# Kernel tuning notes

Measured on AMD Instinct MI355X. Metric: run time of the kernel, lower is better.

## Reference

```python
import jax, jax.numpy as jnp
import numpy as np

B, S, IN, H = 256, 512, 512, 512

def setup_inputs() -> dict:
    key = jax.random.key(0)
    ks = jax.random.split(key, 8)
    s = 1.0 / np.sqrt(H)
    si = 1.0 / np.sqrt(IN)
    return {
        "inputs": jax.random.normal(ks[0], (B, S, IN), dtype=jnp.float32),
        "timestamps": jax.random.uniform(ks[1], (B, S), dtype=jnp.float32),
        "W_all_w": jax.random.uniform(ks[2], (4 * H, H), dtype=jnp.float32, minval=-s, maxval=s),
        "W_all_b": jax.random.uniform(ks[3], (4 * H,), dtype=jnp.float32, minval=-s, maxval=s),
        "U_all_w": jax.random.uniform(ks[4], (4 * H, IN), dtype=jnp.float32, minval=-si, maxval=si),
        "U_all_b": jax.random.uniform(ks[5], (4 * H,), dtype=jnp.float32, minval=-si, maxval=si),
        "W_d_w": jax.random.uniform(ks[6], (H, H), dtype=jnp.float32, minval=-s, maxval=s),
        "W_d_b": jax.random.uniform(ks[7], (H,), dtype=jnp.float32, minval=-s, maxval=s),
    }

def reference(inputs, timestamps, W_all_w, W_all_b, U_all_w, U_all_b, W_d_w, W_d_b):
    b, seq, _ = inputs.shape
    hsz = W_d_w.shape[0]
    # Precompute input projections for all steps at once: [B,S,4H]
    u_proj = jnp.einsum('bsi,gi->bsg', inputs, U_all_w) + U_all_b

    def step(carry, xs):
        h, c = carry
        u_t, t_t = xs  # u_t: [B,4H], t_t: [B]
        c_s1 = jnp.tanh(c @ W_d_w.T + W_d_b)
        c_adj = c - c_s1 + c_s1 * t_t[:, None]
        outs = h @ W_all_w.T + W_all_b + u_t
        f, i, o, c_tmp = jnp.split(outs, 4, axis=1)
        f = jax.nn.sigmoid(f)
        i = jax.nn.sigmoid(i)
        o = jax.nn.sigmoid(o)
        c_tmp = jnp.tanh(c_tmp)
        c = f * c_adj + i * c_tmp
        h = o * jnp.tanh(c)
        return (h, c), (o, h, c)

    h0 = jnp.zeros((b, hsz), dtype=inputs.dtype)
    c0 = jnp.zeros((b, hsz), dtype=inputs.dtype)
    (h, c), (o_seq, h_seq, c_seq) = jax.lax.scan(
        step, (h0, c0),
        (jnp.swapaxes(u_proj, 0, 1), jnp.swapaxes(timestamps, 0, 1)))
    outputs = jnp.swapaxes(o_seq, 0, 1)  # [B,S,H]
    return outputs, h, c
```

## Files before the change

### kernel.cpp

```cpp
#include <hip/hip_runtime.h>
#include <hip/hip_bf16.h>
#include <math.h>

#define BATCH 256
#define SEQ   512
#define IN_D  512
#define HID   512
#define FOURH 2048
#define BS_ROWS (BATCH * SEQ)

typedef __bf16 bf16x8 __attribute__((ext_vector_type(8)));
typedef float  f32x4  __attribute__((ext_vector_type(4)));
typedef unsigned long long ull;

__device__ __forceinline__ float sigf(float x)  { return 1.0f / (1.0f + __expf(-x)); }
__device__ __forceinline__ float tanhf_(float x){ return 1.0f - 2.0f / (__expf(2.0f * x) + 1.0f); }

__global__ __launch_bounds__(256) void init_kernel(
    const float* __restrict__ W_all_w, const float* __restrict__ W_all_b,
    const float* __restrict__ U_all_w, const float* __restrict__ U_all_b,
    const float* __restrict__ W_d_w,
    __bf16* __restrict__ Wb, __bf16* __restrict__ Ub, __bf16* __restrict__ Db,
    float* __restrict__ bias_all,
    unsigned* __restrict__ hc,
    unsigned* __restrict__ bar)
{
    const int stride = gridDim.x * blockDim.x;
    const int tid0 = blockIdx.x * blockDim.x + threadIdx.x;

    const int nW = FOURH * HID;
    for (int i = tid0; i < nW; i += stride) {
        Wb[i] = (__bf16)W_all_w[i];
        Ub[i] = (__bf16)U_all_w[i];
    }
    const int nD = HID * HID;
    for (int i = tid0; i < nD; i += stride) Db[i] = (__bf16)W_d_w[i];
    for (int i = tid0; i < FOURH; i += stride) bias_all[i] = W_all_b[i] + U_all_b[i];
    for (int i = tid0; i < 2 * BATCH * HID; i += stride) hc[i] = 0u;
    for (int i = tid0; i < 256 * 32; i += stride) bar[i] = 0u;
}

__global__ __launch_bounds__(256) void uproj_gemm(
    const float* __restrict__ x, const __bf16* __restrict__ Ub,
    __bf16* __restrict__ up)
{
    const unsigned bid = blockIdx.x;
    const unsigned lg = (bid & 7) * 2048u + (bid >> 3);
    const int cb = lg & 15;
    const int rb = lg >> 4;

    __shared__ __bf16 As[128][64];
    __shared__ __bf16 Bs[128][64];

    const int tid = threadIdx.x;
    const int wave = tid >> 6, lane = tid & 63;
    const int wm = wave >> 1, wn = wave & 1;
    const int lrow = lane & 15, kq = lane >> 4;
    const int sw = (lrow & 7) << 3;

    f32x4 acc[4][4];
    #pragma unroll
    for (int m = 0; m < 4; ++m)
        #pragma unroll
        for (int n = 0; n < 4; ++n) acc[m][n] = (f32x4){0.f, 0.f, 0.f, 0.f};

    const int srow = tid >> 1;
    const int skc  = (tid & 1) * 32;
    const int dsw  = (srow & 7) << 3;

    for (int kk = 0; kk < 512; kk += 64) {
        {
            const float* xs = x + (size_t)(rb * 128 + srow) * 512 + kk + skc;
            #pragma unroll
            for (int j = 0; j < 4; ++j) {
                float4 va = ((const float4*)xs)[2 * j];
                float4 vb = ((const float4*)xs)[2 * j + 1];
                bf16x8 pk;
                pk[0] = (__bf16)va.x; pk[1] = (__bf16)va.y;
                pk[2] = (__bf16)va.z; pk[3] = (__bf16)va.w;
                pk[4] = (__bf16)vb.x; pk[5] = (__bf16)vb.y;
                pk[6] = (__bf16)vb.z; pk[7] = (__bf16)vb.w;
                *(bf16x8*)&As[srow][(skc + j * 8) ^ dsw] = pk;
            }
            const __bf16* bsrc = Ub + (size_t)(cb * 128 + srow) * 512 + kk + skc;
            #pragma unroll
            for (int j = 0; j < 4; ++j)
                *(uint4*)&Bs[srow][(skc + j * 8) ^ dsw] = *(const uint4*)(bsrc + j * 8);
        }
        __syncthreads();

        #pragma unroll
        for (int k2 = 0; k2 < 2; ++k2) {
            const int ke = k2 * 32 + kq * 8;
            bf16x8 af[4], bfr[4];
            #pragma unroll
            for (int m = 0; m < 4; ++m)
                af[m] = *(const bf16x8*)&As[wm * 64 + m * 16 + lrow][ke ^ sw];
            #pragma unroll
            for (int n = 0; n < 4; ++n)
                bfr[n] = *(const bf16x8*)&Bs[wn * 64 + n * 16 + lrow][ke ^ sw];
            #pragma unroll
            for (int m = 0; m < 4; ++m)
                #pragma unroll
                for (int n = 0; n < 4; ++n)
                    acc[m][n] = __builtin_amdgcn_mfma_f32_16x16x32_bf16(af[m], bfr[n], acc[m][n], 0, 0, 0);
        }
        __syncthreads();
    }

    const int colL = lane & 15, r0 = (lane >> 4) * 4;
    const size_t orow0 = (size_t)rb * 128 + wm * 64;
    const int ocol0 = cb * 128 + wn * 64;
    #pragma unroll
    for (int m = 0; m < 4; ++m)
        #pragma unroll
        for (int n = 0; n < 4; ++n)
            #pragma unroll
            for (int i = 0; i < 4; ++i)
                up[(orow0 + m * 16 + r0 + i) * 2048 + ocol0 + n * 16 + colL] = (__bf16)acc[m][n][i];
}

__global__ __launch_bounds__(512) void scan_kernel(
    const __bf16* __restrict__ up,
    const float* __restrict__ timestamps,
    const __bf16* __restrict__ Wb,
    const __bf16* __restrict__ Db,
    const float* __restrict__ bias_all,
    const float* __restrict__ Wd_b,
    unsigned* __restrict__ hc,
    unsigned* __restrict__ bar,
    float* __restrict__ out)
{
    const int tid = threadIdx.x;
    const int bid = blockIdx.x;
    const int bg = bid & 7, hcid = bid >> 3;
    const int b0 = bg * 32;
    const int k0 = hcid * 16;
    const int wave = tid >> 6, lane = tid & 63;
    const int lrow = lane & 15, kq = lane >> 4;
    const int sw = (lrow & 7) << 3;

    __shared__ __bf16 Ah[32][512];
    __shared__ __bf16 Ac[32][512];
    __shared__ float  exg[4 * 2 * 32 * 16];
    __shared__ float  exd[4 * 32 * 16];
    __shared__ __bf16 Us[2][32][64];
    __shared__ float  Ts[2][32];
    __shared__ float  Cm[512];
    __shared__ float  BiasW[64];
    __shared__ float  BiasD[16];

    bf16x8 Bg[2][8];
    bf16x8 Bd[4];
    if (wave < 4) {
        const int kh = wave & 1, pb = wave >> 1;
        #pragma unroll
        for (int uu = 0; uu < 2; ++uu) {
            const int u = pb * 2 + uu;
            #pragma unroll
            for (int ks = 0; ks < 8; ++ks) {
                const int kk = kh * 256 + ks * 32 + kq * 8;
                Bg[uu][ks] = *(const bf16x8*)(Wb + (size_t)(u * 512 + k0 + lrow) * 512 + kk);
            }
        }
    } else {
        const int kq4 = wave - 4;
        #pragma unroll
        for (int ks = 0; ks < 4; ++ks) {
            const int kk = kq4 * 128 + ks * 32 + kq * 8;
            Bd[ks] = *(const bf16x8*)(Db + (size_t)(k0 + lrow) * 512 + kk);
        }
    }

    if (tid < 64) BiasW[tid] = bias_all[(tid >> 4) * 512 + k0 + (tid & 15)];
    else if (tid < 80) BiasD[tid - 64] = Wd_b[k0 + (tid - 64)];
    Cm[tid] = 0.f;
    if (tid < 256) {
        const int row = tid >> 3, j = tid & 7;
        const __bf16* src = up + ((size_t)(b0 + row) * 512 + 0) * 2048
                               + (j >> 1) * 512 + k0 + (j & 1) * 8;
        *(uint4*)&Us[0][row][(j >> 1) * 16 + (j & 1) * 8] = *(const uint4*)src;
    }
    if (tid < 32) Ts[0][tid] = timestamps[(size_t)(b0 + tid) * 512 + 0];
    __syncthreads();

    #pragma unroll 1
    for (int t = 0; t < SEQ; ++t) {
        const int par = t & 1;

        if (t > 0) {
            if (tid < 32) {
                unsigned* fl = &bar[(bg * 32 + tid) * 32];
                while (__hip_atomic_load(fl, __ATOMIC_RELAXED,
                                         __HIP_MEMORY_SCOPE_AGENT) < (unsigned)t)
                    __builtin_amdgcn_s_sleep(2);
            }
            __syncthreads();
        }

        {
            const ull* src = (const ull*)(hc + (size_t)par * BATCH * HID + b0 * 512);
            ull v[16];
            #pragma unroll
            for (int i = 0; i < 16; ++i)
                v[i] = __hip_atomic_load(src + i * 512 + tid, __ATOMIC_RELAXED,
                                         __HIP_MEMORY_SCOPE_AGENT);
            #pragma unroll
            for (int i = 0; i < 16; ++i) {
                const int g = i * 512 + tid;
                const int row = g >> 8;
                const int cp = (g & 255) * 2;
                const unsigned lo = (unsigned)v[i];
                const unsigned hi = (unsigned)(v[i] >> 32);
                const unsigned hp = (lo & 0xFFFFu) | (hi << 16);
                const unsigned cpk = (lo >> 16) | (hi & 0xFFFF0000u);
                const int d = cp ^ ((row & 7) << 3);
                *(unsigned*)&Ah[row][d] = hp;
                *(unsigned*)&Ac[row][d] = cpk;
            }
        }
        __syncthreads();

        uint4 upf;
        float tpf = 0.f;
        const bool do_pf = (t + 1 < SEQ);
        if (do_pf && tid >= 256) {
            const int row = (tid - 256) >> 3, j = (tid - 256) & 7;
            upf = *(const uint4*)(up + ((size_t)(b0 + row) * 512 + (t + 1)) * 2048
                                  + (j >> 1) * 512 + k0 + (j & 1) * 8);
            if (tid < 288) tpf = timestamps[(size_t)(b0 + (tid - 256)) * 512 + (t + 1)];
        }

        if (wave < 4) {
            const int kh = wave & 1, pb = wave >> 1;
            f32x4 acc[2][2];
            #pragma unroll
            for (int uu = 0; uu < 2; ++uu)
                #pragma unroll
                for (int rh = 0; rh < 2; ++rh) acc[uu][rh] = (f32x4){0.f, 0.f, 0.f, 0.f};
            #pragma unroll
            for (int ks = 0; ks < 8; ++ks) {
                const int koff = (kh * 256 + ks * 32 + kq * 8) ^ sw;
                bf16x8 a0 = *(const bf16x8*)&Ah[lrow][koff];
                bf16x8 a1 = *(const bf16x8*)&Ah[16 + lrow][koff];
                #pragma unroll
                for (int uu = 0; uu < 2; ++uu) {
                    acc[uu][0] = __builtin_amdgcn_mfma_f32_16x16x32_bf16(a0, Bg[uu][ks], acc[uu][0], 0, 0, 0);
                    acc[uu][1] = __builtin_amdgcn_mfma_f32_16x16x32_bf16(a1, Bg[uu][ks], acc[uu][1], 0, 0, 0);
                }
            }
            const int colL = lane & 15, r0 = (lane >> 4) * 4;
            #pragma unroll
            for (int uu = 0; uu < 2; ++uu)
                #pragma unroll
                for (int rh = 0; rh < 2; ++rh)
                    #pragma unroll
                    for (int i = 0; i < 4; ++i)
                        exg[(((pb * 2 + uu) * 2 + kh) * 32 + rh * 16 + r0 + i) * 16 + colL] = acc[uu][rh][i];
        } else {
            const int kq4 = wave - 4;
            f32x4 acc0 = {0.f, 0.f, 0.f, 0.f}, acc1 = {0.f, 0.f, 0.f, 0.f};
            #pragma unroll
            for (int ks = 0; ks < 4; ++ks) {
                const int koff = (kq4 * 128 + ks * 32 + kq * 8) ^ sw;
                bf16x8 a0 = *(const bf16x8*)&Ac[lrow][koff];
                bf16x8 a1 = *(const bf16x8*)&Ac[16 + lrow][koff];
                acc0 = __builtin_amdgcn_mfma_f32_16x16x32_bf16(a0, Bd[ks], acc0, 0, 0, 0);
                acc1 = __builtin_amdgcn_mfma_f32_16x16x32_bf16(a1, Bd[ks], acc1, 0, 0, 0);
            }
            const int colL = lane & 15, r0 = (lane >> 4) * 4;
            #pragma unroll
            for (int i = 0; i < 4; ++i) {
                exd[(kq4 * 32 + r0 + i) * 16 + colL]      = acc0[i];
                exd[(kq4 * 32 + 16 + r0 + i) * 16 + colL] = acc1[i];
            }
        }

        if (do_pf && tid >= 256) {
            const int row = (tid - 256) >> 3, j = (tid - 256) & 7;
            *(uint4*)&Us[par ^ 1][row][(j >> 1) * 16 + (j & 1) * 8] = upf;
            if (tid < 288) Ts[par ^ 1][tid - 256] = tpf;
        }
        __syncthreads();

        float o_def = 0.f;
        {
            const int r = tid >> 4, k = tid & 15;
            float g4[4];
            #pragma unroll
            for (int g = 0; g < 4; ++g)
                g4[g] = exg[((g * 2 + 0) * 32 + r) * 16 + k]
                      + exg[((g * 2 + 1) * 32 + r) * 16 + k]
                      + (float)Us[par][r][g * 16 + k] + BiasW[g * 16 + k];
            float dd = BiasD[k];
            #pragma unroll
            for (int q = 0; q < 4; ++q) dd += exd[(q * 32 + r) * 16 + k];

            const float c_old = Cm[tid];
            const float tt = Ts[par][r];
            const float c_s1  = tanhf_(dd);
            const float c_adj = c_old - c_s1 + c_s1 * tt;
            const float f  = sigf(g4[0]);
            const float ii = sigf(g4[1]);
            const float o  = sigf(g4[2]);
            const float c_tmp = tanhf_(g4[3]);
            const float c_new = f * c_adj + ii * c_tmp;
            const float h_new = o * tanhf_(c_new);
            Cm[tid] = c_new;

            if (t == SEQ - 1) {
                __builtin_nontemporal_store(o,
                    &out[((size_t)(b0 + r) * 512 + t) * 512 + k0 + k]);
                const size_t base = (size_t)BATCH * SEQ * HID;
                out[base + (size_t)(b0 + r) * 512 + k0 + k] = h_new;
                out[base + (size_t)BATCH * HID + (size_t)(b0 + r) * 512 + k0 + k] = c_new;
            } else {
                o_def = o;
                const unsigned short hb = __builtin_bit_cast(unsigned short, (__bf16)h_new);
                const unsigned short cb = __builtin_bit_cast(unsigned short, (__bf16)c_new);
                const unsigned pk = (unsigned)hb | ((unsigned)cb << 16);
                unsigned* dst = hc + (size_t)(par ^ 1) * BATCH * HID
                                   + (size_t)(b0 + r) * 512 + k0 + k;
                __hip_atomic_store(dst, pk, __ATOMIC_RELAXED, __HIP_MEMORY_SCOPE_AGENT);
            }
        }
        __syncthreads();

        if (t < SEQ - 1) {
            if (tid == 0)
                __hip_atomic_store(&bar[(bg * 32 + hcid) * 32], (unsigned)(t + 1),
                                   __ATOMIC_RELAXED, __HIP_MEMORY_SCOPE_AGENT);
            {
                const int r = tid >> 4, k = tid & 15;
                __builtin_nontemporal_store(o_def,
                    &out[((size_t)(b0 + r) * 512 + t) * 512 + k0 + k]);
            }
        }
    }
}

extern "C" void kernel_launch(void* const* d_in, const int* in_sizes, int n_in,
                              void* d_out, int out_size, void* d_ws, size_t ws_size,
                              hipStream_t stream) {
    const float* inputs     = (const float*)d_in[0];
    const float* timestamps = (const float*)d_in[1];
    const float* W_all_w    = (const float*)d_in[2];
    const float* W_all_b    = (const float*)d_in[3];
    const float* U_all_w    = (const float*)d_in[4];
    const float* U_all_b    = (const float*)d_in[5];
    const float* W_d_w      = (const float*)d_in[6];
    const float* W_d_b      = (const float*)d_in[7];
    float* out = (float*)d_out;

    char* ws = (char*)d_ws;
    size_t off = 0;
    auto alloc = [&](size_t bytes) -> void* {
        void* p = ws + off;
        off += (bytes + 255) & ~(size_t)255;
        return p;
    };
    __bf16* Wb       = (__bf16*)alloc((size_t)FOURH * HID * 2);
    __bf16* Ub       = (__bf16*)alloc((size_t)FOURH * HID * 2);
    __bf16* Db       = (__bf16*)alloc((size_t)HID * HID * 2);
    float*  bias_all = (float*) alloc((size_t)FOURH * 4);
    unsigned* hcbuf  = (unsigned*)alloc((size_t)2 * BATCH * HID * 4);
    unsigned* bar    = (unsigned*)alloc(256 * 32 * 4);
    __bf16* up       = (__bf16*)alloc((size_t)BS_ROWS * FOURH * 2);

    hipLaunchKernelGGL(init_kernel, dim3(1024), dim3(256), 0, stream,
                       W_all_w, W_all_b, U_all_w, U_all_b, W_d_w,
                       Wb, Ub, Db, bias_all, hcbuf, bar);

    hipLaunchKernelGGL(uproj_gemm, dim3(16384), dim3(256), 0, stream,
                       inputs, Ub, up);

    void* sargs[] = {
        (void*)&up, (void*)&timestamps, (void*)&Wb, (void*)&Db,
        (void*)&bias_all, (void*)&W_d_b,
        (void*)&hcbuf, (void*)&bar, (void*)&out
    };
    hipLaunchCooperativeKernel((const void*)scan_kernel, dim3(256), dim3(512),
                               sargs, 0, stream);
}
```

Measured before the change: 2.585 ms.

## Load recurrent h/c fragments directly from global into MFMA registers, skipping LDS staging

The scan kernel now stores h and c in separate bf16 buffers and has every wave load its MFMA A-fragments straight from global memory into registers. This removes the per-step LDS staging copy and the extra barrier that went with it. The work is also redistributed so all 8 waves handle both the gate GEMM and the decay GEMM, split over K quarters and row halves, and the exchange arrays are padded to stride 17 to avoid bank conflicts. The trade-offs are more global loads per step, more partial sums to reduce, and h/c stores paired through lane shuffles.

Result: slower. 3.784 ms (+46.4%).

```diff
diff --git a/kernel.cpp b/kernel.cpp
--- a/kernel.cpp
+++ b/kernel.cpp
@@ -11,10 +11,13 @@
 
 typedef __bf16 bf16x8 __attribute__((ext_vector_type(8)));
 typedef float  f32x4  __attribute__((ext_vector_type(4)));
+typedef unsigned uint32x4 __attribute__((ext_vector_type(4)));
 typedef unsigned long long ull;
 
 __device__ __forceinline__ float sigf(float x)  { return 1.0f / (1.0f + __expf(-x)); }
 __device__ __forceinline__ float tanhf_(float x){ return 1.0f - 2.0f / (__expf(2.0f * x) + 1.0f); }
+
+union frag_cvt { ull u[2]; bf16x8 v; };
 
 __global__ __launch_bounds__(256) void init_kernel(
     const float* __restrict__ W_all_w, const float* __restrict__ W_all_b,
@@ -22,7 +25,8 @@
     const float* __restrict__ W_d_w,
     __bf16* __restrict__ Wb, __bf16* __restrict__ Ub, __bf16* __restrict__ Db,
     float* __restrict__ bias_all,
-    unsigned* __restrict__ hc,
+    unsigned* __restrict__ hz,
+    unsigned* __restrict__ cz,
     unsigned* __restrict__ bar)
 {
     const int stride = gridDim.x * blockDim.x;
@@ -36,7 +40,8 @@
     const int nD = HID * HID;
     for (int i = tid0; i < nD; i += stride) Db[i] = (__bf16)W_d_w[i];
     for (int i = tid0; i < FOURH; i += stride) bias_all[i] = W_all_b[i] + U_all_b[i];
-    for (int i = tid0; i < 2 * BATCH * HID; i += stride) hc[i] = 0u;
+    const int nH = BATCH * HID;
+    for (int i = tid0; i < nH; i += stride) { hz[i] = 0u; cz[i] = 0u; }
     for (int i = tid0; i < 256 * 32; i += stride) bar[i] = 0u;
 }
 
@@ -127,7 +132,8 @@
     const __bf16* __restrict__ Db,
     const float* __restrict__ bias_all,
     const float* __restrict__ Wd_b,
-    unsigned* __restrict__ hc,
+    __bf16* __restrict__ hbuf,
+    __bf16* __restrict__ cbuf,
     unsigned* __restrict__ bar,
     float* __restrict__ out)
 {
@@ -138,39 +144,26 @@
     const int k0 = hcid * 16;
     const int wave = tid >> 6, lane = tid & 63;
     const int lrow = lane & 15, kq = lane >> 4;
-    const int sw = (lrow & 7) << 3;
-
-    __shared__ __bf16 Ah[32][512];
-    __shared__ __bf16 Ac[32][512];
-    __shared__ float  exg[4 * 2 * 32 * 16];
-    __shared__ float  exd[4 * 32 * 16];
+    const int rh = wave >> 2, kq4 = wave & 3;
+    const int kb = kq4 * 128 + kq * 8;
+
+    __shared__ float  exg[16 * 32 * 17];
+    __shared__ float  exd[4 * 32 * 17];
     __shared__ __bf16 Us[2][32][64];
     __shared__ float  Ts[2][32];
     __shared__ float  Cm[512];
     __shared__ float  BiasW[64];
     __shared__ float  BiasD[16];
 
-    bf16x8 Bg[2][8];
-    bf16x8 Bd[4];
-    if (wave < 4) {
-        const int kh = wave & 1, pb = wave >> 1;
-        #pragma unroll
-        for (int uu = 0; uu < 2; ++uu) {
-            const int u = pb * 2 + uu;
-            #pragma unroll
-            for (int ks = 0; ks < 8; ++ks) {
-                const int kk = kh * 256 + ks * 32 + kq * 8;
-                Bg[uu][ks] = *(const bf16x8*)(Wb + (size_t)(u * 512 + k0 + lrow) * 512 + kk);
-            }
-        }
-    } else {
-        const int kq4 = wave - 4;
-        #pragma unroll
-        for (int ks = 0; ks < 4; ++ks) {
-            const int kk = kq4 * 128 + ks * 32 + kq * 8;
-            Bd[ks] = *(const bf16x8*)(Db + (size_t)(k0 + lrow) * 512 + kk);
-        }
-    }
+    bf16x8 Bg[4][4], Bd4[4];
+    #pragma unroll
+    for (int u = 0; u < 4; ++u)
+        #pragma unroll
+        for (int ks = 0; ks < 4; ++ks)
+            Bg[u][ks] = *(const bf16x8*)(Wb + (size_t)(u * 512 + k0 + lrow) * 512 + kb + ks * 32);
+    #pragma unroll
+    for (int ks = 0; ks < 4; ++ks)
+        Bd4[ks] = *(const bf16x8*)(Db + (size_t)(k0 + lrow) * 512 + kb + ks * 32);
 
     if (tid < 64) BiasW[tid] = bias_all[(tid >> 4) * 512 + k0 + (tid & 15)];
     else if (tid < 80) BiasD[tid - 64] = Wd_b[k0 + (tid - 64)];
@@ -184,6 +177,8 @@
     if (tid < 32) Ts[0][tid] = timestamps[(size_t)(b0 + tid) * 512 + 0];
     __syncthreads();
 
+    const int arow = b0 + rh * 16 + lrow;
+
     #pragma unroll 1
     for (int t = 0; t < SEQ; ++t) {
         const int par = t & 1;
@@ -193,93 +188,67 @@
                 unsigned* fl = &bar[(bg * 32 + tid) * 32];
                 while (__hip_atomic_load(fl, __ATOMIC_RELAXED,
                                          __HIP_MEMORY_SCOPE_AGENT) < (unsigned)t)
-                    __builtin_amdgcn_s_sleep(2);
+                    __builtin_amdgcn_s_sleep(1);
             }
             __syncthreads();
         }
 
-        {
-            const ull* src = (const ull*)(hc + (size_t)par * BATCH * HID + b0 * 512);
-            ull v[16];
-            #pragma unroll
-            for (int i = 0; i < 16; ++i)
-                v[i] = __hip_atomic_load(src + i * 512 + tid, __ATOMIC_RELAXED,
-                                         __HIP_MEMORY_SCOPE_AGENT);
-            #pragma unroll
-            for (int i = 0; i < 16; ++i) {
-                const int g = i * 512 + tid;
-                const int row = g >> 8;
-                const int cp = (g & 255) * 2;
-                const unsigned lo = (unsigned)v[i];
-                const unsigned hi = (unsigned)(v[i] >> 32);
-                const unsigned hp = (lo & 0xFFFFu) | (hi << 16);
-                const unsigned cpk = (lo >> 16) | (hi & 0xFFFF0000u);
-                const int d = cp ^ ((row & 7) << 3);
-                *(unsigned*)&Ah[row][d] = hp;
-                *(unsigned*)&Ac[row][d] = cpk;
-            }
-        }
-        __syncthreads();
-
-        uint4 upf;
+        const __bf16* hs = hbuf + (size_t)par * BATCH * HID;
+        const __bf16* cs = cbuf + (size_t)par * BATCH * HID;
+        const size_t abase = (size_t)arow * 512 + kb;
+        ull ahv[4][2], acv[4][2];
+        #pragma unroll
+        for (int ks = 0; ks < 4; ++ks) {
+            const ull* ph = (const ull*)(hs + abase + ks * 32);
+            const ull* pc = (const ull*)(cs + abase + ks * 32);
+            ahv[ks][0] = __hip_atomic_load(ph,     __ATOMIC_RELAXED, __HIP_MEMORY_SCOPE_AGENT);
+            ahv[ks][1] = __hip_atomic_load(ph + 1, __ATOMIC_RELAXED, __HIP_MEMORY_SCOPE_AGENT);
+            acv[ks][0] = __hip_atomic_load(pc,     __ATOMIC_RELAXED, __HIP_MEMORY_SCOPE_AGENT);
+            acv[ks][1] = __hip_atomic_load(pc + 1, __ATOMIC_RELAXED, __HIP_MEMORY_SCOPE_AGENT);
+        }
+
+        uint32x4 upf;
         float tpf = 0.f;
         const bool do_pf = (t + 1 < SEQ);
-        if (do_pf && tid >= 256) {
-            const int row = (tid - 256) >> 3, j = (tid - 256) & 7;
-            upf = *(const uint4*)(up + ((size_t)(b0 + row) * 512 + (t + 1)) * 2048
-                                  + (j >> 1) * 512 + k0 + (j & 1) * 8);
-            if (tid < 288) tpf = timestamps[(size_t)(b0 + (tid - 256)) * 512 + (t + 1)];
-        }
-
-        if (wave < 4) {
-            const int kh = wave & 1, pb = wave >> 1;
-            f32x4 acc[2][2];
-            #pragma unroll
-            for (int uu = 0; uu < 2; ++uu)
+        if (do_pf && tid < 256) {
+            const int row = tid >> 3, j = tid & 7;
+            upf = __builtin_nontemporal_load(
+                (const uint32x4*)(up + ((size_t)(b0 + row) * 512 + (t + 1)) * 2048
+                                  + (j >> 1) * 512 + k0 + (j & 1) * 8));
+        }
+        if (do_pf && tid < 32) tpf = timestamps[(size_t)(b0 + tid) * 512 + (t + 1)];
+
+        f32x4 ag[4], ad;
+        #pragma unroll
+        for (int u = 0; u < 4; ++u) ag[u] = (f32x4){0.f, 0.f, 0.f, 0.f};
+        ad = (f32x4){0.f, 0.f, 0.f, 0.f};
+        #pragma unroll
+        for (int ks = 0; ks < 4; ++ks) {
+            frag_cvt fh; fh.u[0] = ahv[ks][0]; fh.u[1] = ahv[ks][1];
+            #pragma unroll
+            for (int u = 0; u < 4; ++u)
+                ag[u] = __builtin_amdgcn_mfma_f32_16x16x32_bf16(fh.v, Bg[u][ks], ag[u], 0, 0, 0);
+            frag_cvt fc; fc.u[0] = acv[ks][0]; fc.u[1] = acv[ks][1];
+            ad = __builtin_amdgcn_mfma_f32_16x16x32_bf16(fc.v, Bd4[ks], ad, 0, 0, 0);
+        }
+
+        if (do_pf && tid < 256) {
+            const int row = tid >> 3, j = tid & 7;
+            *(uint32x4*)&Us[par ^ 1][row][(j >> 1) * 16 + (j & 1) * 8] = upf;
+        }
+        if (do_pf && tid < 32) Ts[par ^ 1][tid] = tpf;
+
+        {
+            const int colL = lane & 15, r0 = (lane >> 4) * 4;
+            const int rbase = rh * 16 + r0;
+            #pragma unroll
+            for (int u = 0; u < 4; ++u)
                 #pragma unroll
-                for (int rh = 0; rh < 2; ++rh) acc[uu][rh] = (f32x4){0.f, 0.f, 0.f, 0.f};
-            #pragma unroll
-            for (int ks = 0; ks < 8; ++ks) {
-                const int koff = (kh * 256 + ks * 32 + kq * 8) ^ sw;
-                bf16x8 a0 = *(const bf16x8*)&Ah[lrow][koff];
-                bf16x8 a1 = *(const bf16x8*)&Ah[16 + lrow][koff];
-                #pragma unroll
-                for (int uu = 0; uu < 2; ++uu) {
-                    acc[uu][0] = __builtin_amdgcn_mfma_f32_16x16x32_bf16(a0, Bg[uu][ks], acc[uu][0], 0, 0, 0);
-                    acc[uu][1] = __builtin_amdgcn_mfma_f32_16x16x32_bf16(a1, Bg[uu][ks], acc[uu][1], 0, 0, 0);
-                }
-            }
-            const int colL = lane & 15, r0 = (lane >> 4) * 4;
-            #pragma unroll
-            for (int uu = 0; uu < 2; ++uu)
-                #pragma unroll
-                for (int rh = 0; rh < 2; ++rh)
-                    #pragma unroll
-                    for (int i = 0; i < 4; ++i)
-                        exg[(((pb * 2 + uu) * 2 + kh) * 32 + rh * 16 + r0 + i) * 16 + colL] = acc[uu][rh][i];
-        } else {
-            const int kq4 = wave - 4;
-            f32x4 acc0 = {0.f, 0.f, 0.f, 0.f}, acc1 = {0.f, 0.f, 0.f, 0.f};
-            #pragma unroll
-            for (int ks = 0; ks < 4; ++ks) {
-                const int koff = (kq4 * 128 + ks * 32 + kq * 8) ^ sw;
-                bf16x8 a0 = *(const bf16x8*)&Ac[lrow][koff];
-                bf16x8 a1 = *(const bf16x8*)&Ac[16 + lrow][koff];
-                acc0 = __builtin_amdgcn_mfma_f32_16x16x32_bf16(a0, Bd[ks], acc0, 0, 0, 0);
-                acc1 = __builtin_amdgcn_mfma_f32_16x16x32_bf16(a1, Bd[ks], acc1, 0, 0, 0);
-            }
-            const int colL = lane & 15, r0 = (lane >> 4) * 4;
-            #pragma unroll
-            for (int i = 0; i < 4; ++i) {
-                exd[(kq4 * 32 + r0 + i) * 16 + colL]      = acc0[i];
-                exd[(kq4 * 32 + 16 + r0 + i) * 16 + colL] = acc1[i];
-            }
-        }
-
-        if (do_pf && tid >= 256) {
-            const int row = (tid - 256) >> 3, j = (tid - 256) & 7;
-            *(uint4*)&Us[par ^ 1][row][(j >> 1) * 16 + (j & 1) * 8] = upf;
-            if (tid < 288) Ts[par ^ 1][tid - 256] = tpf;
+                for (int i = 0; i < 4; ++i)
+                    exg[((u * 4 + kq4) * 32 + rbase + i) * 17 + colL] = ag[u][i];
+            #pragma unroll
+            for (int i = 0; i < 4; ++i)
+                exd[(kq4 * 32 + rbase + i) * 17 + colL] = ad[i];
         }
         __syncthreads();
 
@@ -289,12 +258,14 @@
             float g4[4];
             #pragma unroll
             for (int g = 0; g < 4; ++g)
-                g4[g] = exg[((g * 2 + 0) * 32 + r) * 16 + k]
-                      + exg[((g * 2 + 1) * 32 + r) * 16 + k]
-                      + (float)Us[par][r][g * 16 + k] + BiasW[g * 16 + k];
-            float dd = BiasD[k];
-            #pragma unroll
-            for (int q = 0; q < 4; ++q) dd += exd[(q * 32 + r) * 16 + k];
+                g4[g] = BiasW[g * 16 + k] + (float)Us[par][r][g * 16 + k]
+                      + exg[((g * 4 + 0) * 32 + r) * 17 + k]
+                      + exg[((g * 4 + 1) * 32 + r) * 17 + k]
+                      + exg[((g * 4 + 2) * 32 + r) * 17 + k]
+                      + exg[((g * 4 + 3) * 32 + r) * 17 + k];
+            float dd = BiasD[k]
+                     + exd[(0 * 32 + r) * 17 + k] + exd[(1 * 32 + r) * 17 + k]
+                     + exd[(2 * 32 + r) * 17 + k] + exd[(3 * 32 + r) * 17 + k];
 
             const float c_old = Cm[tid];
             const float tt = Ts[par][r];
@@ -308,6 +279,11 @@
             const float h_new = o * tanhf_(c_new);
             Cm[tid] = c_new;
 
+            const unsigned hb16 = (unsigned)__builtin_bit_cast(unsigned short, (__bf16)h_new);
+            const unsigned cb16 = (unsigned)__builtin_bit_cast(unsigned short, (__bf16)c_new);
+            const unsigned hn = (unsigned)__shfl_xor((int)hb16, 1);
+            const unsigned cn = (unsigned)__shfl_xor((int)cb16, 1);
+
             if (t == SEQ - 1) {
                 __builtin_nontemporal_store(o,
                     &out[((size_t)(b0 + r) * 512 + t) * 512 + k0 + k]);
@@ -316,12 +292,15 @@
                 out[base + (size_t)BATCH * HID + (size_t)(b0 + r) * 512 + k0 + k] = c_new;
             } else {
                 o_def = o;
-                const unsigned short hb = __builtin_bit_cast(unsigned short, (__bf16)h_new);
-                const unsigned short cb = __builtin_bit_cast(unsigned short, (__bf16)c_new);
-                const unsigned pk = (unsigned)hb | ((unsigned)cb << 16);
-                unsigned* dst = hc + (size_t)(par ^ 1) * BATCH * HID
-                                   + (size_t)(b0 + r) * 512 + k0 + k;
-                __hip_atomic_store(dst, pk, __ATOMIC_RELAXED, __HIP_MEMORY_SCOPE_AGENT);
+                if (!(lane & 1)) {
+                    const unsigned hp = hb16 | (hn << 16);
+                    const unsigned cp = cb16 | (cn << 16);
+                    const size_t e = ((size_t)(b0 + r) * 512 + k0 + k) >> 1;
+                    unsigned* hd = (unsigned*)(hbuf + (size_t)(par ^ 1) * BATCH * HID);
+                    unsigned* cd = (unsigned*)(cbuf + (size_t)(par ^ 1) * BATCH * HID);
+                    __hip_atomic_store(hd + e, hp, __ATOMIC_RELAXED, __HIP_MEMORY_SCOPE_AGENT);
+                    __hip_atomic_store(cd + e, cp, __ATOMIC_RELAXED, __HIP_MEMORY_SCOPE_AGENT);
+                }
             }
         }
         __syncthreads();
@@ -363,13 +342,15 @@
     __bf16* Ub       = (__bf16*)alloc((size_t)FOURH * HID * 2);
     __bf16* Db       = (__bf16*)alloc((size_t)HID * HID * 2);
     float*  bias_all = (float*) alloc((size_t)FOURH * 4);
-    unsigned* hcbuf  = (unsigned*)alloc((size_t)2 * BATCH * HID * 4);
+    __bf16* hbuf     = (__bf16*)alloc((size_t)2 * BATCH * HID * 2);
+    __bf16* cbuf     = (__bf16*)alloc((size_t)2 * BATCH * HID * 2);
     unsigned* bar    = (unsigned*)alloc(256 * 32 * 4);
     __bf16* up       = (__bf16*)alloc((size_t)BS_ROWS * FOURH * 2);
 
     hipLaunchKernelGGL(init_kernel, dim3(1024), dim3(256), 0, stream,
                        W_all_w, W_all_b, U_all_w, U_all_b, W_d_w,
-                       Wb, Ub, Db, bias_all, hcbuf, bar);
+                       Wb, Ub, Db, bias_all,
+                       (unsigned*)hbuf, (unsigned*)cbuf, bar);
 
     hipLaunchKernelGGL(uproj_gemm, dim3(16384), dim3(256), 0, stream,
                        inputs, Ub, up);
@@ -377,7 +358,7 @@
     void* sargs[] = {
         (void*)&up, (void*)&timestamps, (void*)&Wb, (void*)&Db,
         (void*)&bias_all, (void*)&W_d_b,
-        (void*)&hcbuf, (void*)&bar, (void*)&out
+        (void*)&hbuf, (void*)&cbuf, (void*)&bar, (void*)&out
     };
     hipLaunchCooperativeKernel((const void*)scan_kernel, dim3(256), dim3(512),
                                sargs, 0, stream);
```
